# Kernel tuning notes

Measured on AMD Instinct MI355X. Metric: run time of the kernel, lower is better.

Reference implementation:

```python
import jax, jax.numpy as jnp
import numpy as np

B, C, H, W = 32, 128, 56, 56
KSEL = 2            # gate columns (experts selected per sample)
E = 8               # expert_per_task
KN = 128            # kernel_num
KS = 3              # kernel_size
PAD = (KS - 1) // 2


def setup_inputs() -> dict:
    key = jax.random.key(0)
    k1, k2, k3, k4 = jax.random.split(key, 4)
    x = jax.random.normal(k1, (B, C, H, W), dtype=jnp.float32)
    gate = jax.random.randint(k2, (B, KSEL), 0, E, dtype=jnp.int32)
    conv_special_param = jax.random.normal(k3, (E, KN, C, KS, KS), dtype=jnp.float32) * 0.05
    conv_channel_param = jax.random.normal(k4, (E, C, C + KN, 1, 1), dtype=jnp.float32) * 0.05
    return {"x": x, "gate": gate,
            "conv_special_param": conv_special_param,
            "conv_channel_param": conv_channel_param}


def _per_sample_conv(xb, wb):
    # xb: [C, H+2p, W+2p], wb: [KN, C, KS, KS] -> [KN, H, W]
    out = jax.lax.conv_general_dilated(
        xb[None], wb, window_strides=(1, 1), padding='VALID',
        dimension_numbers=('NCHW', 'OIHW', 'NCHW'))
    return out[0]


def reference(x, gate, conv_special_param, conv_channel_param):
    px = jnp.pad(x, ((0, 0), (0, 0), (PAD, PAD), (PAD, PAD)))

    def per_gate(idx):  # idx: [B] expert indices for this gate column
        w_spec = conv_special_param[idx]                 # [B, KN, C, KS, KS]
        nf = jax.vmap(_per_sample_conv)(px, w_spec)      # [B, KN, H, W]
        cated = jnp.concatenate([x, nf], axis=1)         # [B, C+KN, H, W]
        w_ch = conv_channel_param[idx][..., 0, 0]        # [B, C, C+KN]
        return jnp.einsum('boc,bchw->bohw', w_ch, cated)  # [B, C, H, W]

    # stack over gate columns -> [B, KSEL, C, H, W]
    return jax.vmap(per_gate, in_axes=1, out_axes=1)(gate)
```

## Files before the change

### kernel.cpp

```cpp
#include <hip/hip_runtime.h>
#include <hip/hip_bf16.h>

#define B_   32
#define C_   128
#define H_   56
#define W_   56
#define KSEL 2
#define E_   8
#define KN_  128

typedef __attribute__((ext_vector_type(8))) short short8;
typedef __attribute__((ext_vector_type(4))) float f32x4;

static __device__ __forceinline__ ushort f2bf(float f) {
  union { float f; uint u; } v; v.f = f;
  uint u = v.u;
  return (ushort)((u + 0x7fffu + ((u >> 16) & 1u)) >> 16);
}

__global__ __launch_bounds__(256) void prep_x_kernel(
    const float* __restrict__ x, ushort* __restrict__ xh) {
  const int hp = blockIdx.x;
  const int b  = blockIdx.y;
  const int tid = threadIdx.x;
  ushort* rowp = xh + (size_t)(b * 58 + hp) * 58 * 128;

  if (hp == 0 || hp == 57) {
    uint4 z = make_uint4(0, 0, 0, 0);
    for (int l = tid; l < 464; l += 256) ((uint4*)rowp)[l] = z;
    return;
  }
  const int h = hp - 1;
  __shared__ __align__(16) ushort sT[56 * 136];

  const float* xb = x + (size_t)b * C_ * H_ * W_ + h * W_;
#pragma unroll
  for (int it = 0; it < 7; ++it) {
    int i4 = tid + it * 256;
    int c  = i4 / 14;
    int w4 = (i4 - c * 14) * 4;
    float4 v = *(const float4*)(xb + (size_t)c * (H_ * W_) + w4);
    sT[(w4 + 0) * 136 + c] = f2bf(v.x);
    sT[(w4 + 1) * 136 + c] = f2bf(v.y);
    sT[(w4 + 2) * 136 + c] = f2bf(v.z);
    sT[(w4 + 3) * 136 + c] = f2bf(v.w);
  }
  __syncthreads();
  for (int l = tid; l < 896; l += 256) {
    int w = l >> 4, sub = l & 15;
    uint4 v = *(const uint4*)&sT[w * 136 + sub * 8];
    *(uint4*)(rowp + (size_t)(w + 1) * 128 + sub * 8) = v;
  }
  if (tid < 32) {
    int wp = (tid < 16) ? 0 : 57;
    uint4 z = make_uint4(0, 0, 0, 0);
    *(uint4*)(rowp + (size_t)wp * 128 + (tid & 15) * 8) = z;
  }
}

__global__ __launch_bounds__(256) void fuse_weights_kernel(
    const float* __restrict__ Ws,
    const float* __restrict__ Wch,
    ushort* __restrict__ Weff) {
  const int e  = blockIdx.x;
  const int o0 = blockIdx.y * 32;
  const int c0 = blockIdx.z * 32;
  const int tid = threadIdx.x;
  const int ol = tid >> 3;
  const int cq = (tid & 7) * 4;

  __shared__ __align__(16) float sA[32 * 129];
  __shared__ __align__(16) float sB[32 * 32 * 12];

#pragma unroll
  for (int it = 0; it < 4; ++it) {
    int i4 = tid + it * 256;
    int o  = i4 >> 5;
    int kk = (i4 & 31) * 4;
    float4 v = *(const float4*)(Wch + (size_t)(e * C_ + o0 + o) * 256 + 128 + kk);
    sA[o * 129 + kk + 0] = v.x;
    sA[o * 129 + kk + 1] = v.y;
    sA[o * 129 + kk + 2] = v.z;
    sA[o * 129 + kk + 3] = v.w;
  }

  float acc[9][4];
#pragma unroll
  for (int j = 0; j < 9; ++j)
#pragma unroll
    for (int c2 = 0; c2 < 4; ++c2) acc[j][c2] = 0.f;

  for (int k0 = 0; k0 < 128; k0 += 32) {
    __syncthreads();
    {
      int k = tid >> 3, seg = tid & 7;
      const float* src = Ws + ((size_t)(e * KN_ + k0 + k) * C_ + c0) * 9 + seg * 36;
      float vb[36];
#pragma unroll
      for (int q = 0; q < 9; ++q) {
        float4 v = *(const float4*)(src + q * 4);
        vb[q * 4 + 0] = v.x; vb[q * 4 + 1] = v.y;
        vb[q * 4 + 2] = v.z; vb[q * 4 + 3] = v.w;
      }
      int c = seg * 4, j = 0;
#pragma unroll
      for (int m = 0; m < 36; ++m) {
        sB[(k * 32 + c) * 12 + j] = vb[m];
        if (++j == 9) { j = 0; ++c; }
      }
    }
    __syncthreads();
    for (int k = 0; k < 32; ++k) {
      float a = sA[ol * 129 + k0 + k];
#pragma unroll
      for (int c2 = 0; c2 < 4; ++c2) {
        const float* bp = &sB[(k * 32 + cq + c2) * 12];
#pragma unroll
        for (int j = 0; j < 9; ++j) acc[j][c2] += a * bp[j];
      }
    }
  }

  const int o = o0 + ol;
#pragma unroll
  for (int c2 = 0; c2 < 4; ++c2)
    acc[4][c2] += Wch[(size_t)(e * C_ + o) * 256 + c0 + cq + c2];
#pragma unroll
  for (int j = 0; j < 9; ++j) {
    uint lo = (uint)f2bf(acc[j][0]) | ((uint)f2bf(acc[j][1]) << 16);
    uint hi = (uint)f2bf(acc[j][2]) | ((uint)f2bf(acc[j][3]) << 16);
    uint2* dst = (uint2*)(Weff + ((size_t)((e * 9 + j) * KN_ + o)) * C_ + c0 + cq);
    *dst = make_uint2(lo, hi);
  }
}

#define XSTR 40
#define WSTR 40

__global__ __launch_bounds__(256, 2) void conv_mfma_kernel(
    const ushort* __restrict__ xh,
    const int* __restrict__ gate,
    const ushort* __restrict__ Weff,
    float* __restrict__ out) {
  const int ht = blockIdx.x;
  const int bg = blockIdx.y;
  const int b  = bg >> 1;
  const int h0 = ht * 4;
  const int e  = gate[bg];

  const int tid = threadIdx.x;
  const int wv = tid >> 6, lane = tid & 63;
  const int l15 = lane & 15, kq = lane >> 4;
  const int mh = wv >> 1, nh = wv & 1;

  __shared__ __align__(16) ushort sX[6 * 58 * XSTR];
  __shared__ __align__(16) ushort sW[3 * 128 * WSTR];

  f32x4 acc[7][4];
#pragma unroll
  for (int t = 0; t < 7; ++t)
#pragma unroll
    for (int i = 0; i < 4; ++i) acc[t][i] = (f32x4){0.f, 0.f, 0.f, 0.f};

  int addr0[7];
#pragma unroll
  for (int t = 0; t < 7; ++t) {
    int p = mh * 112 + t * 16 + l15;
    int r = p / 56;
    int w = p - r * 56;
    addr0[t] = (r * 58 + w) * XSTR + kq * 8;
  }
  int woff[4];
#pragma unroll
  for (int i = 0; i < 4; ++i) woff[i] = (nh * 64 + i * 16 + l15) * WSTR + kq * 8;

  const ushort* xb = xh + (size_t)b * 58 * 58 * 128;
  const ushort* wb = Weff + (size_t)e * 9 * KN_ * C_;

  for (int cc = 0; cc < 4; ++cc) {
    const int c0 = cc * 32;
    __syncthreads();
    for (int l = tid; l < 1392; l += 256) {
      int row = l / 232;
      int rem = l - row * 232;
      int col = rem >> 2, sub = rem & 3;
      uint4 v = *(const uint4*)(xb + ((size_t)(h0 + row) * 58 + col) * 128 + c0 + sub * 8);
      *(uint4*)&sX[(row * 58 + col) * XSTR + sub * 8] = v;
    }
    for (int dy = 0; dy < 3; ++dy) {
      __syncthreads();
      {
        int l = tid;
#pragma unroll
        for (int it = 0; it < 6; ++it, l += 256) {
          int sub = l & 3, o = (l >> 2) & 127, dx = l >> 9;
          uint4 v = *(const uint4*)(wb + (size_t)((dy * 3 + dx) * KN_ + o) * C_ + c0 + sub * 8);
          *(uint4*)&sW[(dx * 128 + o) * WSTR + sub * 8] = v;
        }
      }
      __syncthreads();
#pragma unroll
      for (int dx = 0; dx < 3; ++dx) {
        short8 bfr[4];
#pragma unroll
        for (int i = 0; i < 4; ++i)
          bfr[i] = *(const short8*)&sW[woff[i] + dx * 128 * WSTR];
        const int ao = (dy * 58 + dx) * XSTR;
#pragma unroll
        for (int t = 0; t < 7; ++t) {
          short8 a = *(const short8*)&sX[addr0[t] + ao];
#pragma unroll
          for (int i = 0; i < 4; ++i)
            acc[t][i] = __builtin_amdgcn_mfma_f32_16x16x32_bf16(a, bfr[i], acc[t][i], 0, 0, 0);
        }
      }
    }
  }

#pragma unroll
  for (int t = 0; t < 7; ++t) {
    int p0 = mh * 112 + t * 16 + kq * 4;
    int r  = p0 / 56;
    int w0 = p0 - r * 56;
    int h  = h0 + r;
#pragma unroll
    for (int i = 0; i < 4; ++i) {
      int o = nh * 64 + i * 16 + l15;
      float* op = out + (((size_t)bg * C_ + o) * H_ + h) * W_ + w0;
      *(float4*)op = make_float4(acc[t][i][0], acc[t][i][1], acc[t][i][2], acc[t][i][3]);
    }
  }
}

extern "C" void kernel_launch(void* const* d_in, const int* in_sizes, int n_in,
                              void* d_out, int out_size, void* d_ws, size_t ws_size,
                              hipStream_t stream) {
  const float* x    = (const float*)d_in[0];
  const int*   gate = (const int*)d_in[1];
  const float* Ws   = (const float*)d_in[2];
  const float* Wch  = (const float*)d_in[3];
  float* out = (float*)d_out;

  ushort* xh   = (ushort*)d_ws;
  ushort* Weff = xh + (size_t)32 * 58 * 58 * 128;

  dim3 g0(58, 32);
  prep_x_kernel<<<g0, 256, 0, stream>>>(x, xh);

  dim3 g1(8, 4, 4);
  fuse_weights_kernel<<<g1, 256, 0, stream>>>(Ws, Wch, Weff);

  dim3 g2(14, 64);
  conv_mfma_kernel<<<g2, 256, 0, stream>>>(xh, gate, Weff, out);
}
```

Baseline: 252.3 us.

## Pre-swizzle fused weights into MFMA fragment layout and load directly from global

The weight-fusion kernel now writes Weff in a per-lane MFMA B-fragment order, so the conv kernel loads each fragment with one 16-byte global read instead of staging weights through LDS. This removes the sW buffer and two barriers per dy step, shrinking LDS use and raising the occupancy hint to three blocks per CU. The grid is also flattened and remapped so blocks for the same batch sample fall on the same XCD, which should help L2 reuse of the activation rows. The cost is that weight fragments are now read from L2/global on every dx step with no LDS reuse across waves.

```diff
diff --git a/kernel.cpp b/kernel.cpp
--- a/kernel.cpp
+++ b/kernel.cpp
@@ -125,28 +125,37 @@
 #pragma unroll
   for (int c2 = 0; c2 < 4; ++c2)
     acc[4][c2] += Wch[(size_t)(e * C_ + o) * 256 + c0 + cq + c2];
+
+  const int nt   = (o0 >> 4) + (ol >> 4);
+  const int lane = ((cq >> 3) << 4) | (ol & 15);
 #pragma unroll
   for (int j = 0; j < 9; ++j) {
     uint lo = (uint)f2bf(acc[j][0]) | ((uint)f2bf(acc[j][1]) << 16);
     uint hi = (uint)f2bf(acc[j][2]) | ((uint)f2bf(acc[j][3]) << 16);
-    uint2* dst = (uint2*)(Weff + ((size_t)((e * 9 + j) * KN_ + o)) * C_ + c0 + cq);
-    *dst = make_uint2(lo, hi);
+    size_t base = ((((size_t)(e * 9 + j) * 8 + nt) * 4 + blockIdx.z) * 64 + lane) * 8
+                  + (cq & 4);
+    *(uint2*)(Weff + base) = make_uint2(lo, hi);
   }
 }
 
 #define XSTR 40
-#define WSTR 40
-
-__global__ __launch_bounds__(256, 2) void conv_mfma_kernel(
+
+__global__ __launch_bounds__(256, 3) void conv_mfma_kernel(
     const ushort* __restrict__ xh,
     const int* __restrict__ gate,
     const ushort* __restrict__ Weff,
     float* __restrict__ out) {
-  const int ht = blockIdx.x;
-  const int bg = blockIdx.y;
-  const int b  = bg >> 1;
-  const int h0 = ht * 4;
-  const int e  = gate[bg];
+  const int P   = blockIdx.x;
+  const int xcd = P & 7;
+  const int s   = P >> 3;
+  const int bl  = s / 28;
+  const int r1  = s - bl * 28;
+  const int g   = r1 / 14;
+  const int ht  = r1 - g * 14;
+  const int b   = xcd * 4 + bl;
+  const int bg  = b * 2 + g;
+  const int h0  = ht * 4;
+  const int e   = gate[bg];
 
   const int tid = threadIdx.x;
   const int wv = tid >> 6, lane = tid & 63;
@@ -154,7 +163,6 @@
   const int mh = wv >> 1, nh = wv & 1;
 
   __shared__ __align__(16) ushort sX[6 * 58 * XSTR];
-  __shared__ __align__(16) ushort sW[3 * 128 * WSTR];
 
   f32x4 acc[7][4];
 #pragma unroll
@@ -170,12 +178,11 @@
     int w = p - r * 56;
     addr0[t] = (r * 58 + w) * XSTR + kq * 8;
   }
-  int woff[4];
-#pragma unroll
-  for (int i = 0; i < 4; ++i) woff[i] = (nh * 64 + i * 16 + l15) * WSTR + kq * 8;
 
   const ushort* xb = xh + (size_t)b * 58 * 58 * 128;
-  const ushort* wb = Weff + (size_t)e * 9 * KN_ * C_;
+  const ushort* wlane = Weff + (size_t)e * (9 * 8 * 4 * 64 * 8)
+                             + (size_t)(nh * 4) * (4 * 64 * 8)
+                             + (size_t)lane * 8;
 
   for (int cc = 0; cc < 4; ++cc) {
     const int c0 = cc * 32;
@@ -187,24 +194,18 @@
       uint4 v = *(const uint4*)(xb + ((size_t)(h0 + row) * 58 + col) * 128 + c0 + sub * 8);
       *(uint4*)&sX[(row * 58 + col) * XSTR + sub * 8] = v;
     }
+    __syncthreads();
+#pragma unroll
     for (int dy = 0; dy < 3; ++dy) {
-      __syncthreads();
-      {
-        int l = tid;
-#pragma unroll
-        for (int it = 0; it < 6; ++it, l += 256) {
-          int sub = l & 3, o = (l >> 2) & 127, dx = l >> 9;
-          uint4 v = *(const uint4*)(wb + (size_t)((dy * 3 + dx) * KN_ + o) * C_ + c0 + sub * 8);
-          *(uint4*)&sW[(dx * 128 + o) * WSTR + sub * 8] = v;
-        }
-      }
-      __syncthreads();
 #pragma unroll
       for (int dx = 0; dx < 3; ++dx) {
+        const int j = dy * 3 + dx;
         short8 bfr[4];
 #pragma unroll
         for (int i = 0; i < 4; ++i)
-          bfr[i] = *(const short8*)&sW[woff[i] + dx * 128 * WSTR];
+          bfr[i] = *(const short8*)(wlane + (size_t)j * (8 * 4 * 64 * 8)
+                                          + (size_t)i * (4 * 64 * 8)
+                                          + (size_t)cc * (64 * 8));
         const int ao = (dy * 58 + dx) * XSTR;
 #pragma unroll
         for (int t = 0; t < 7; ++t) {
@@ -250,6 +251,6 @@
   dim3 g1(8, 4, 4);
   fuse_weights_kernel<<<g1, 256, 0, stream>>>(Ws, Wch, Weff);
 
-  dim3 g2(14, 64);
+  dim3 g2(896);
   conv_mfma_kernel<<<g2, 256, 0, stream>>>(xh, gate, Weff, out);
 }
```

Result: slower. 284.6 us (+12.8%).
